# Kernel optimization log

Measured on AMD Instinct MI355X. Metric: run time of the kernel, lower is better.

Reference implementation:

```python
import jax, jax.numpy as jnp
import numpy as np

B, T, I, H = 32, 1024, 512, 512


def setup_inputs() -> dict:
    key = jax.random.key(0)
    ks = jax.random.split(key, 9)
    s = 0.05  # xavier-ish scale for 512-dim layers
    return {
        "x": jax.random.normal(ks[0], (B, T, I), jnp.float32),
        "W_in_0": jax.random.normal(ks[1], (I, H), jnp.float32) * s,
        "b_in_0": jnp.zeros((H,), jnp.float32),
        "W_h_0": jax.random.normal(ks[2], (H, 2 * H), jnp.float32) * s,
        "b_h_0": jnp.zeros((2 * H,), jnp.float32),
        "W_in_1": jax.random.normal(ks[3], (H, H), jnp.float32) * s,
        "b_in_1": jnp.zeros((H,), jnp.float32),
        "W_h_1": jax.random.normal(ks[4], (H, 2 * H), jnp.float32) * s,
        "b_h_1": jnp.zeros((2 * H,), jnp.float32),
    }


def _cell(ti, m_prev, c_prev, W_h, b_h, hid):
    # ti: transformed input [B,H]; gates from previous m (the "hidden")
    gates = m_prev @ W_h + b_h                 # [B,2H]
    retain = jax.nn.sigmoid(gates[:, :hid])
    merge = jax.nn.sigmoid(gates[:, hid:])
    c_next = jnp.tanh(c_prev + retain * ti)
    m_next = (1.0 - merge) * ti + merge * c_next
    return m_next, c_next


def reference(x, W_in_0, b_in_0, W_h_0, b_h_0, W_in_1, b_in_1, W_h_1, b_h_1):
    b, t, _ = x.shape
    hid = W_in_0.shape[1]
    # layer-0 input transform is independent of the recurrence: batch it over time
    ti0_all = jnp.swapaxes(x @ W_in_0 + b_in_0, 0, 1)  # [T,B,H]

    def step(carry, ti0):
        (m0, c0), (m1, c1) = carry
        m0n, c0n = _cell(ti0, m0, c0, W_h_0, b_h_0, hid)
        ti1 = m0n @ W_in_1 + b_in_1
        m1n, c1n = _cell(ti1, m1, c1, W_h_1, b_h_1, hid)
        out_t = jnp.stack([m0n, m1n], axis=1)  # [B,L,H]
        return ((m0n, c0n), (m1n, c1n)), out_t

    z = jnp.zeros((b, hid), x.dtype)
    init = ((z, z), (z, z))
    (h0, h1), outs = jax.lax.scan(step, init, ti0_all)
    output = jnp.swapaxes(outs, 0, 1)  # [B,T,L,H]
    final_c = jnp.stack([h0[1], h1[1]], axis=1)  # [B,L,H]
    con = jnp.broadcast_to(final_c[:, None], output.shape)  # [B,T,L,H]
    return (output, output, con)
```

## Files before the change

### kernel.cpp

```cpp
#include <hip/hip_runtime.h>


#define T_STEPS 1024

typedef __bf16 bf8 __attribute__((ext_vector_type(8)));
typedef float  f4  __attribute__((ext_vector_type(4)));
typedef unsigned u32x4 __attribute__((ext_vector_type(4)));

__device__ __forceinline__ f4 mfma16(bf8 a, bf8 b, f4 c) {
    return __builtin_amdgcn_mfma_f32_16x16x32_bf16(a, b, c, 0, 0, 0);
}
__device__ __forceinline__ float sigf(float x)     { return 1.f / (1.f + __expf(-x)); }
__device__ __forceinline__ float tanhfast(float x) { return 1.f - 2.f / (1.f + __expf(2.f * x)); }
__device__ __forceinline__ unsigned pack2(float lo, float hi) {
    union { __bf16 h; unsigned short u; } a, b;
    a.h = (__bf16)lo; b.h = (__bf16)hi;
    return ((unsigned)b.u << 16) | (unsigned)a.u;
}
__device__ __forceinline__ void wait_lds_ge(int* p, int tgt) {
    while (__hip_atomic_load(p, __ATOMIC_ACQUIRE, __HIP_MEMORY_SCOPE_WORKGROUP) < tgt)
        __builtin_amdgcn_s_sleep(1);
}
__device__ __forceinline__ void set_lds(int* p, int v) {
    __hip_atomic_store(p, v, __ATOMIC_RELEASE, __HIP_MEMORY_SCOPE_WORKGROUP);
}


__global__ __launch_bounds__(256) void k_init(const float* __restrict__ x,
                                              const float* __restrict__ w_in0,
                                              __bf16* __restrict__ xbf,
                                              __bf16* __restrict__ w0hi,
                                              __bf16* __restrict__ w0lo,
                                              unsigned* __restrict__ ws)
{
    size_t id = (size_t)blockIdx.x * 256 + threadIdx.x;
    size_t gs = (size_t)gridDim.x * 256;
    for (size_t i = id; i < 33024; i += gs) ws[i] = 0u;
    for (size_t i = id; i < (size_t)16777216; i += gs) {
        size_t r = i >> 9, c = i & 511;
        size_t b = r & 31, t = r >> 5;
        xbf[i] = (__bf16)x[(((b << 10) + t) << 9) + c];
    }
    for (size_t i = id; i < (size_t)262144; i += gs) {
        size_t n = i >> 9, k = i & 511;
        float v = w_in0[(k << 9) + n];
        __bf16 h = (__bf16)v;
        w0hi[i] = h;
        w0lo[i] = (__bf16)(v - (float)h);
    }
}

__global__ __launch_bounds__(256) void k_pregemm(const __bf16* __restrict__ xbf,
                                                 const __bf16* __restrict__ w0hi,
                                                 const __bf16* __restrict__ w0lo,
                                                 const float* __restrict__ b_in0,
                                                 float* __restrict__ ti0)
{
    int tid = threadIdx.x, lane = tid & 63, wid = tid >> 6;
    int wg = blockIdx.x;
    int mbase = (wg & 511) * 64 + wid * 16;
    int nbase = (wg >> 9) * 128;
    int col = lane & 15, kgrp = lane >> 4;
    f4 acc[8];
#pragma unroll
    for (int i = 0; i < 8; ++i) acc[i] = (f4){0.f, 0.f, 0.f, 0.f};
    const __bf16* ap = xbf + (size_t)(mbase + col) * 512 + kgrp * 8;
    for (int kk = 0; kk < 16; ++kk) {
        bf8 a = *reinterpret_cast<const bf8*>(ap + kk * 32);
        const __bf16* wb = w0hi + (size_t)(nbase + col) * 512 + kk * 32 + kgrp * 8;
        const __bf16* wl = w0lo + (size_t)(nbase + col) * 512 + kk * 32 + kgrp * 8;
#pragma unroll
        for (int ct = 0; ct < 8; ++ct) {
            bf8 bh = *reinterpret_cast<const bf8*>(wb + (size_t)ct * 16 * 512);
            bf8 bl = *reinterpret_cast<const bf8*>(wl + (size_t)ct * 16 * 512);
            acc[ct] = mfma16(a, bh, acc[ct]);
            acc[ct] = mfma16(a, bl, acc[ct]);
        }
    }
#pragma unroll
    for (int ct = 0; ct < 8; ++ct) {
        int c = nbase + ct * 16 + col;
        float bias = b_in0[c];
#pragma unroll
        for (int r = 0; r < 4; ++r) {
            int row = mbase + kgrp * 4 + r;
            ti0[(size_t)row * 512 + c] = acc[ct][r] + bias;
        }
    }
}

__global__ __launch_bounds__(192, 1) void k_recur(
    const float* __restrict__ wh0, const float* __restrict__ bh0g,
    const float* __restrict__ win1, const float* __restrict__ bin1g,
    const float* __restrict__ wh1, const float* __restrict__ bh1g,
    const float* __restrict__ ti0,
    float* __restrict__ out,
    unsigned* __restrict__ ws)
{
    __shared__ __bf16 sW[9][8192];
    __shared__ float  sTi1[2][256];
    __shared__ float  sMn[2][256];
    __shared__ float  sB[5][16];
    __shared__ int    sAready, sAout, sBdone, sCdone;

    int tid = threadIdx.x, lane = tid & 63, wid = tid >> 6;
    int wg = blockIdx.x;
    int rank  = wg & 31;
    int mhalf = wg >> 5;

    unsigned* flagsA = ws + mhalf * 64;
    unsigned* flagsB = ws + 128 + mhalf * 64;
    unsigned* ring0d = ws + 256;
    unsigned* ring1d = ws + 256 + 16384;
    float* fc = (float*)(ws + 33024);

    int h0 = rank * 16;
    int col = lane & 15, kgrp = lane >> 4;
    int rbrow = mhalf * 16;

    for (int i = tid; i < 8192; i += 192) {
        int cl = i & 15, k = i >> 4;
        int sw = (cl * 512 + k) ^ ((cl & 7) << 3);
        float v0r = wh0[(size_t)k * 1024 + h0 + cl];
        float v0m = wh0[(size_t)k * 1024 + 512 + h0 + cl];
        float v1r = wh1[(size_t)k * 1024 + h0 + cl];
        float v1m = wh1[(size_t)k * 1024 + 512 + h0 + cl];
        float vt  = win1[(size_t)k * 512 + h0 + cl];
        __bf16 a;
        a = (__bf16)v0r; sW[0][sw] = a; sW[1][sw] = (__bf16)(v0r - (float)a);
        a = (__bf16)v0m; sW[2][sw] = a; sW[3][sw] = (__bf16)(v0m - (float)a);
        a = (__bf16)v1r; sW[4][sw] = a; sW[5][sw] = (__bf16)(v1r - (float)a);
        a = (__bf16)v1m; sW[6][sw] = a; sW[7][sw] = (__bf16)(v1m - (float)a);
        sW[8][sw] = (__bf16)vt;
    }
    if (tid < 16) {
        sB[0][tid] = bh0g[h0 + tid];
        sB[1][tid] = bh0g[512 + h0 + tid];
        sB[2][tid] = bh1g[h0 + tid];
        sB[3][tid] = bh1g[512 + h0 + tid];
        sB[4][tid] = bin1g[h0 + tid];
    }
    if (tid == 0) { sAready = -1; sAout = -1; sBdone = -1; sCdone = -1; }
    __syncthreads();

    float cs[4] = {0.f, 0.f, 0.f, 0.f};

    if (wid == 0) {
#pragma unroll 1
        for (int ph = 0; ph <= T_STEPS; ++ph) {
            float t0v[4] = {0.f, 0.f, 0.f, 0.f};
            if (ph < T_STEPS) {
#pragma unroll
                for (int r = 0; r < 4; ++r)
                    t0v[r] = ti0[((size_t)ph * 32 + rbrow + kgrp * 4 + r) * 512 + h0 + col];
            }
            if (ph > 0) {
                const unsigned tgt = (unsigned)ph;
                const unsigned* fp = flagsA + (lane & 31);
                while (true) {
                    unsigned v = __hip_atomic_load(fp, __ATOMIC_RELAXED,
                                                   __HIP_MEMORY_SCOPE_AGENT);
                    if (__ballot(v >= tgt) == ~0ull) break;
                    __builtin_amdgcn_s_sleep(1);
                }
                __builtin_amdgcn_sched_barrier(0);
            }
            u32x4 au[16];
            {
                const unsigned* rp = ring0d + ((ph + 1) & 1) * 8192 + (rbrow + col) * 256 + kgrp * 4;
#pragma unroll
                for (int kk = 0; kk < 16; ++kk)
                    asm volatile("global_load_dwordx4 %0, %1, off sc1"
                                 : "=v"(au[kk]) : "v"(rp + kk * 16));
                asm volatile("s_waitcnt vmcnt(0)" ::: "memory");
            }
            f4 accR = {0.f, 0.f, 0.f, 0.f};
            f4 accM = {0.f, 0.f, 0.f, 0.f};
            f4 accT = {0.f, 0.f, 0.f, 0.f};
#pragma unroll
            for (int kk = 0; kk < 16; ++kk) {
                union { u32x4 u; bf8 v; } A;
                A.u = au[kk];
                int e = (col * 512 + kk * 32 + kgrp * 8) ^ ((col & 7) << 3);
                accR = mfma16(A.v, *reinterpret_cast<const bf8*>(&sW[0][e]), accR);
                accR = mfma16(A.v, *reinterpret_cast<const bf8*>(&sW[1][e]), accR);
                accM = mfma16(A.v, *reinterpret_cast<const bf8*>(&sW[2][e]), accM);
                accM = mfma16(A.v, *reinterpret_cast<const bf8*>(&sW[3][e]), accM);
                accT = mfma16(A.v, *reinterpret_cast<const bf8*>(&sW[8][e]), accT);
            }
            wait_lds_ge(&sBdone, ph - 2);
#pragma unroll
            for (int r = 0; r < 4; ++r)
                sTi1[ph & 1][(kgrp * 4 + r) * 16 + col] = accT[r] + sB[4][col];
            if (lane == 0) set_lds(&sAready, ph);

            if (ph < T_STEPS) {
                float mn[4];
#pragma unroll
                for (int r = 0; r < 4; ++r) {
                    float retain = sigf(accR[r] + sB[0][col]);
                    float merge  = sigf(accM[r] + sB[1][col]);
                    float cv = tanhfast(cs[r] + retain * t0v[r]);
                    cs[r] = cv;
                    mn[r] = (1.f - merge) * t0v[r] + merge * cv;
                }
#pragma unroll
                for (int r = 0; r < 4; ++r) {
                    float hi = __shfl_xor(mn[r], 1, 64);
                    if (!(col & 1)) {
                        int grow = rbrow + kgrp * 4 + r;
                        __hip_atomic_store(&ring0d[(ph & 1) * 8192 + grow * 256 + rank * 8 + (col >> 1)],
                                           pack2(mn[r], hi), __ATOMIC_RELAXED,
                                           __HIP_MEMORY_SCOPE_AGENT);
                    }
                }
                asm volatile("s_waitcnt vmcnt(0)" ::: "memory");
                if (lane == 0)
                    __hip_atomic_store(&flagsA[rank], (unsigned)(ph + 1), __ATOMIC_RELAXED,
                                       __HIP_MEMORY_SCOPE_AGENT);
                wait_lds_ge(&sCdone, ph - 2);
#pragma unroll
                for (int r = 0; r < 4; ++r)
                    sMn[ph & 1][(kgrp * 4 + r) * 16 + col] = mn[r];
                if (lane == 0) set_lds(&sAout, ph);
            }
        }
#pragma unroll
        for (int r = 0; r < 4; ++r) {
            int b = rbrow + kgrp * 4 + r;
            fc[((size_t)b * 2 + 0) * 512 + h0 + col] = cs[r];
        }
    } else if (wid == 1) {
#pragma unroll 1
        for (int ph = 1; ph <= T_STEPS; ++ph) {
            if (ph >= 2) {
                const unsigned tgt = (unsigned)(ph - 1);
                const unsigned* fp = flagsB + (lane & 31);
                while (true) {
                    unsigned v = __hip_atomic_load(fp, __ATOMIC_RELAXED,
                                                   __HIP_MEMORY_SCOPE_AGENT);
                    if (__ballot(v >= tgt) == ~0ull) break;
                    __builtin_amdgcn_s_sleep(1);
                }
                __builtin_amdgcn_sched_barrier(0);
            }
            u32x4 au[16];
            {
                const unsigned* rp = ring1d + (ph & 1) * 8192 + (rbrow + col) * 256 + kgrp * 4;
#pragma unroll
                for (int kk = 0; kk < 16; ++kk)
                    asm volatile("global_load_dwordx4 %0, %1, off sc1"
                                 : "=v"(au[kk]) : "v"(rp + kk * 16));
                asm volatile("s_waitcnt vmcnt(0)" ::: "memory");
            }
            f4 accR = {0.f, 0.f, 0.f, 0.f};
            f4 accM = {0.f, 0.f, 0.f, 0.f};
#pragma unroll
            for (int kk = 0; kk < 16; ++kk) {
                union { u32x4 u; bf8 v; } A;
                A.u = au[kk];
                int e = (col * 512 + kk * 32 + kgrp * 8) ^ ((col & 7) << 3);
                accR = mfma16(A.v, *reinterpret_cast<const bf8*>(&sW[4][e]), accR);
                accR = mfma16(A.v, *reinterpret_cast<const bf8*>(&sW[5][e]), accR);
                accM = mfma16(A.v, *reinterpret_cast<const bf8*>(&sW[6][e]), accM);
                accM = mfma16(A.v, *reinterpret_cast<const bf8*>(&sW[7][e]), accM);
            }
            wait_lds_ge(&sAready, ph);
            float mn[4];
#pragma unroll
            for (int r = 0; r < 4; ++r) {
                float t1v = sTi1[ph & 1][(kgrp * 4 + r) * 16 + col];
                float retain = sigf(accR[r] + sB[2][col]);
                float merge  = sigf(accM[r] + sB[3][col]);
                float cv = tanhfast(cs[r] + retain * t1v);
                cs[r] = cv;
                mn[r] = (1.f - merge) * t1v + merge * cv;
            }
            if (lane == 0) set_lds(&sBdone, ph);
#pragma unroll
            for (int r = 0; r < 4; ++r) {
                float hi = __shfl_xor(mn[r], 1, 64);
                if (!(col & 1)) {
                    int grow = rbrow + kgrp * 4 + r;
                    __hip_atomic_store(&ring1d[((ph + 1) & 1) * 8192 + grow * 256 + rank * 8 + (col >> 1)],
                                       pack2(mn[r], hi), __ATOMIC_RELAXED,
                                       __HIP_MEMORY_SCOPE_AGENT);
                }
            }
            asm volatile("s_waitcnt vmcnt(0)" ::: "memory");
            if (lane == 0)
                __hip_atomic_store(&flagsB[rank], (unsigned)ph, __ATOMIC_RELAXED,
                                   __HIP_MEMORY_SCOPE_AGENT);
#pragma unroll
            for (int r = 0; r < 4; ++r) {
                int b = rbrow + kgrp * 4 + r;
                size_t ob = ((size_t)b * 1024 + (ph - 1)) * 1024 + 512 + h0 + col;
                __builtin_nontemporal_store(mn[r], out + ob);
                __builtin_nontemporal_store(mn[r], out + (size_t)33554432 + ob);
            }
        }
#pragma unroll
        for (int r = 0; r < 4; ++r) {
            int b = rbrow + kgrp * 4 + r;
            fc[((size_t)b * 2 + 1) * 512 + h0 + col] = cs[r];
        }
    } else {
#pragma unroll 1
        for (int ph = 0; ph < T_STEPS; ++ph) {
            wait_lds_ge(&sAout, ph);
            float mn[4];
#pragma unroll
            for (int r = 0; r < 4; ++r)
                mn[r] = sMn[ph & 1][(kgrp * 4 + r) * 16 + col];
            if (lane == 0) set_lds(&sCdone, ph);
#pragma unroll
            for (int r = 0; r < 4; ++r) {
                int b = rbrow + kgrp * 4 + r;
                size_t ob = ((size_t)b * 1024 + ph) * 1024 + h0 + col;
                __builtin_nontemporal_store(mn[r], out + ob);
                __builtin_nontemporal_store(mn[r], out + (size_t)33554432 + ob);
            }
        }
    }
}

__global__ __launch_bounds__(256) void k_final(const float* __restrict__ fc,
                                               float* __restrict__ seg2)
{
    size_t id = (size_t)blockIdx.x * 256 + threadIdx.x;
    size_t gs = (size_t)gridDim.x * 256;
    for (size_t i = id; i < (size_t)8388608; i += gs) {
        size_t flat = i * 4;
        int h = (int)(flat & 511);
        int l = (int)((flat >> 9) & 1);
        int b = (int)(flat >> 20);
        f4 v = *reinterpret_cast<const f4*>(&fc[((size_t)b * 2 + l) * 512 + h]);
        *reinterpret_cast<f4*>(&seg2[flat]) = v;
    }
}

extern "C" void kernel_launch(void* const* d_in, const int* in_sizes, int n_in,
                              void* d_out, int out_size, void* d_ws, size_t ws_size,
                              hipStream_t stream)
{
    const float* x     = (const float*)d_in[0];
    const float* w_in0 = (const float*)d_in[1];
    const float* b_in0 = (const float*)d_in[2];
    const float* wh0   = (const float*)d_in[3];
    const float* bh0   = (const float*)d_in[4];
    const float* win1  = (const float*)d_in[5];
    const float* bin1  = (const float*)d_in[6];
    const float* wh1   = (const float*)d_in[7];
    const float* bh1   = (const float*)d_in[8];
    float* out = (float*)d_out;

    float*  seg2 = out + (size_t)2 * 33554432;
    float*  ti0  = seg2;
    __bf16* xbf  = (__bf16*)(ti0 + 16777216);
    __bf16* w0hi = xbf + 16777216;
    __bf16* w0lo = w0hi + 262144;

    k_init<<<1024, 256, 0, stream>>>(x, w_in0, xbf, w0hi, w0lo, (unsigned*)d_ws);
    k_pregemm<<<2048, 256, 0, stream>>>(xbf, w0hi, w0lo, b_in0, ti0);
    k_recur<<<64, 192, 0, stream>>>(wh0, bh0, win1, bin1, wh1, bh1, ti0, out,
                                    (unsigned*)d_ws);
    k_final<<<1024, 256, 0, stream>>>((const float*)((unsigned*)d_ws + 33024), seg2);
}
```

Measured before the change: 5.325 ms.

## Replace flag-based inter-block sync with step-tagged ring entries; offload layer-1 stores

Result: slower. 7.572 ms (+42.2%).

```diff
diff --git a/kernel.cpp b/kernel.cpp
--- a/kernel.cpp
+++ b/kernel.cpp
@@ -31,11 +31,11 @@
                                               __bf16* __restrict__ xbf,
                                               __bf16* __restrict__ w0hi,
                                               __bf16* __restrict__ w0lo,
-                                              unsigned* __restrict__ ws)
+                                              unsigned* __restrict__ ringz)
 {
     size_t id = (size_t)blockIdx.x * 256 + threadIdx.x;
     size_t gs = (size_t)gridDim.x * 256;
-    for (size_t i = id; i < 33024; i += gs) ws[i] = 0u;
+    for (size_t i = id; i < 65536; i += gs) ringz[i] = 0u;
     for (size_t i = id; i < (size_t)16777216; i += gs) {
         size_t r = i >> 9, c = i & 511;
         size_t b = r & 31, t = r >> 5;
@@ -89,30 +89,60 @@
     }
 }
 
+__device__ __forceinline__ void pull_ring(const unsigned long long* rp, unsigned tg,
+                                          bf8* afr)
+{
+    while (true) {
+        u32x4 au[32];
+#pragma unroll
+        for (int kk = 0; kk < 16; ++kk) {
+            asm volatile("global_load_dwordx4 %0, %1, off sc1"
+                         : "=v"(au[2 * kk]) : "v"(rp + (size_t)kk * 16));
+            asm volatile("global_load_dwordx4 %0, %1, off sc1"
+                         : "=v"(au[2 * kk + 1]) : "v"(rp + (size_t)kk * 16 + 2));
+        }
+        asm volatile("s_waitcnt vmcnt(0)" ::: "memory");
+        __builtin_amdgcn_sched_barrier(0);
+        unsigned bad = 0;
+#pragma unroll
+        for (int i = 0; i < 32; ++i) bad |= (au[i][1] ^ tg) | (au[i][3] ^ tg);
+        if (__ballot(bad == 0) == ~0ull) {
+#pragma unroll
+            for (int kk = 0; kk < 16; ++kk) {
+                union { u32x4 u; bf8 v; } A;
+                A.u = (u32x4){au[2 * kk][0], au[2 * kk][2],
+                              au[2 * kk + 1][0], au[2 * kk + 1][2]};
+                afr[kk] = A.v;
+            }
+            return;
+        }
+        __builtin_amdgcn_s_sleep(1);
+    }
+}
+
 __global__ __launch_bounds__(192, 1) void k_recur(
     const float* __restrict__ wh0, const float* __restrict__ bh0g,
     const float* __restrict__ win1, const float* __restrict__ bin1g,
     const float* __restrict__ wh1, const float* __restrict__ bh1g,
     const float* __restrict__ ti0,
     float* __restrict__ out,
-    unsigned* __restrict__ ws)
+    float* __restrict__ fc,
+    unsigned long long* __restrict__ ringbase)
 {
     __shared__ __bf16 sW[9][8192];
     __shared__ float  sTi1[2][256];
-    __shared__ float  sMn[2][256];
+    __shared__ float  sMn0[2][256];
+    __shared__ float  sMn1[2][256];
     __shared__ float  sB[5][16];
-    __shared__ int    sAready, sAout, sBdone, sCdone;
+    __shared__ int    sAready, sAout, sB1rdy, sBdone, sCdone;
 
     int tid = threadIdx.x, lane = tid & 63, wid = tid >> 6;
     int wg = blockIdx.x;
     int rank  = wg & 31;
     int mhalf = wg >> 5;
 
-    unsigned* flagsA = ws + mhalf * 64;
-    unsigned* flagsB = ws + 128 + mhalf * 64;
-    unsigned* ring0d = ws + 256;
-    unsigned* ring1d = ws + 256 + 16384;
-    float* fc = (float*)(ws + 33024);
+    unsigned long long* ring0t = ringbase;
+    unsigned long long* ring1t = ringbase + 16384;
 
     int h0 = rank * 16;
     int col = lane & 15, kgrp = lane >> 4;
@@ -140,7 +170,7 @@
         sB[3][tid] = bh1g[512 + h0 + tid];
         sB[4][tid] = bin1g[h0 + tid];
     }
-    if (tid == 0) { sAready = -1; sAout = -1; sBdone = -1; sCdone = -1; }
+    if (tid == 0) { sAready = -1; sAout = -1; sB1rdy = -1; sBdone = -1; sCdone = -1; }
     __syncthreads();
 
     float cs[4] = {0.f, 0.f, 0.f, 0.f};
@@ -154,39 +184,20 @@
                 for (int r = 0; r < 4; ++r)
                     t0v[r] = ti0[((size_t)ph * 32 + rbrow + kgrp * 4 + r) * 512 + h0 + col];
             }
-            if (ph > 0) {
-                const unsigned tgt = (unsigned)ph;
-                const unsigned* fp = flagsA + (lane & 31);
-                while (true) {
-                    unsigned v = __hip_atomic_load(fp, __ATOMIC_RELAXED,
-                                                   __HIP_MEMORY_SCOPE_AGENT);
-                    if (__ballot(v >= tgt) == ~0ull) break;
-                    __builtin_amdgcn_s_sleep(1);
-                }
-                __builtin_amdgcn_sched_barrier(0);
-            }
-            u32x4 au[16];
-            {
-                const unsigned* rp = ring0d + ((ph + 1) & 1) * 8192 + (rbrow + col) * 256 + kgrp * 4;
-#pragma unroll
-                for (int kk = 0; kk < 16; ++kk)
-                    asm volatile("global_load_dwordx4 %0, %1, off sc1"
-                                 : "=v"(au[kk]) : "v"(rp + kk * 16));
-                asm volatile("s_waitcnt vmcnt(0)" ::: "memory");
-            }
+            bf8 afr[16];
+            pull_ring(ring0t + ((ph + 1) & 1) * 8192 + (size_t)(rbrow + col) * 256 + kgrp * 4,
+                      (unsigned)ph, afr);
             f4 accR = {0.f, 0.f, 0.f, 0.f};
             f4 accM = {0.f, 0.f, 0.f, 0.f};
             f4 accT = {0.f, 0.f, 0.f, 0.f};
 #pragma unroll
             for (int kk = 0; kk < 16; ++kk) {
-                union { u32x4 u; bf8 v; } A;
-                A.u = au[kk];
                 int e = (col * 512 + kk * 32 + kgrp * 8) ^ ((col & 7) << 3);
-                accR = mfma16(A.v, *reinterpret_cast<const bf8*>(&sW[0][e]), accR);
-                accR = mfma16(A.v, *reinterpret_cast<const bf8*>(&sW[1][e]), accR);
-                accM = mfma16(A.v, *reinterpret_cast<const bf8*>(&sW[2][e]), accM);
-                accM = mfma16(A.v, *reinterpret_cast<const bf8*>(&sW[3][e]), accM);
-                accT = mfma16(A.v, *reinterpret_cast<const bf8*>(&sW[8][e]), accT);
+                accR = mfma16(afr[kk], *reinterpret_cast<const bf8*>(&sW[0][e]), accR);
+                accR = mfma16(afr[kk], *reinterpret_cast<const bf8*>(&sW[1][e]), accR);
+                accM = mfma16(afr[kk], *reinterpret_cast<const bf8*>(&sW[2][e]), accM);
+                accM = mfma16(afr[kk], *reinterpret_cast<const bf8*>(&sW[3][e]), accM);
+                accT = mfma16(afr[kk], *reinterpret_cast<const bf8*>(&sW[8][e]), accT);
             }
             wait_lds_ge(&sBdone, ph - 2);
 #pragma unroll
@@ -204,24 +215,21 @@
                     cs[r] = cv;
                     mn[r] = (1.f - merge) * t0v[r] + merge * cv;
                 }
+                unsigned tg1 = (unsigned)(ph + 1);
 #pragma unroll
                 for (int r = 0; r < 4; ++r) {
                     float hi = __shfl_xor(mn[r], 1, 64);
                     if (!(col & 1)) {
                         int grow = rbrow + kgrp * 4 + r;
-                        __hip_atomic_store(&ring0d[(ph & 1) * 8192 + grow * 256 + rank * 8 + (col >> 1)],
-                                           pack2(mn[r], hi), __ATOMIC_RELAXED,
-                                           __HIP_MEMORY_SCOPE_AGENT);
+                        unsigned long long w = ((unsigned long long)tg1 << 32) | pack2(mn[r], hi);
+                        __hip_atomic_store(&ring0t[(ph & 1) * 8192 + (size_t)grow * 256 + rank * 8 + (col >> 1)],
+                                           w, __ATOMIC_RELAXED, __HIP_MEMORY_SCOPE_AGENT);
                     }
                 }
-                asm volatile("s_waitcnt vmcnt(0)" ::: "memory");
-                if (lane == 0)
-                    __hip_atomic_store(&flagsA[rank], (unsigned)(ph + 1), __ATOMIC_RELAXED,
-                                       __HIP_MEMORY_SCOPE_AGENT);
                 wait_lds_ge(&sCdone, ph - 2);
 #pragma unroll
                 for (int r = 0; r < 4; ++r)
-                    sMn[ph & 1][(kgrp * 4 + r) * 16 + col] = mn[r];
+                    sMn0[ph & 1][(kgrp * 4 + r) * 16 + col] = mn[r];
                 if (lane == 0) set_lds(&sAout, ph);
             }
         }
@@ -233,71 +241,50 @@
     } else if (wid == 1) {
 #pragma unroll 1
         for (int ph = 1; ph <= T_STEPS; ++ph) {
-            if (ph >= 2) {
-                const unsigned tgt = (unsigned)(ph - 1);
-                const unsigned* fp = flagsB + (lane & 31);
-                while (true) {
-                    unsigned v = __hip_atomic_load(fp, __ATOMIC_RELAXED,
-                                                   __HIP_MEMORY_SCOPE_AGENT);
-                    if (__ballot(v >= tgt) == ~0ull) break;
-                    __builtin_amdgcn_s_sleep(1);
-                }
-                __builtin_amdgcn_sched_barrier(0);
-            }
-            u32x4 au[16];
-            {
-                const unsigned* rp = ring1d + (ph & 1) * 8192 + (rbrow + col) * 256 + kgrp * 4;
-#pragma unroll
-                for (int kk = 0; kk < 16; ++kk)
-                    asm volatile("global_load_dwordx4 %0, %1, off sc1"
-                                 : "=v"(au[kk]) : "v"(rp + kk * 16));
-                asm volatile("s_waitcnt vmcnt(0)" ::: "memory");
-            }
+            bf8 afr[16];
+            pull_ring(ring1t + (ph & 1) * 8192 + (size_t)(rbrow + col) * 256 + kgrp * 4,
+                      (unsigned)(ph - 1), afr);
             f4 accR = {0.f, 0.f, 0.f, 0.f};
             f4 accM = {0.f, 0.f, 0.f, 0.f};
 #pragma unroll
             for (int kk = 0; kk < 16; ++kk) {
-                union { u32x4 u; bf8 v; } A;
-                A.u = au[kk];
                 int e = (col * 512 + kk * 32 + kgrp * 8) ^ ((col & 7) << 3);
-                accR = mfma16(A.v, *reinterpret_cast<const bf8*>(&sW[4][e]), accR);
-                accR = mfma16(A.v, *reinterpret_cast<const bf8*>(&sW[5][e]), accR);
-                accM = mfma16(A.v, *reinterpret_cast<const bf8*>(&sW[6][e]), accM);
-                accM = mfma16(A.v, *reinterpret_cast<const bf8*>(&sW[7][e]), accM);
+                accR = mfma16(afr[kk], *reinterpret_cast<const bf8*>(&sW[4][e]), accR);
+                accR = mfma16(afr[kk], *reinterpret_cast<const bf8*>(&sW[5][e]), accR);
+                accM = mfma16(afr[kk], *reinterpret_cast<const bf8*>(&sW[6][e]), accM);
+                accM = mfma16(afr[kk], *reinterpret_cast<const bf8*>(&sW[7][e]), accM);
             }
             wait_lds_ge(&sAready, ph);
+            float t1v[4];
+#pragma unroll
+            for (int r = 0; r < 4; ++r)
+                t1v[r] = sTi1[ph & 1][(kgrp * 4 + r) * 16 + col];
+            if (lane == 0) set_lds(&sBdone, ph);
             float mn[4];
 #pragma unroll
             for (int r = 0; r < 4; ++r) {
-                float t1v = sTi1[ph & 1][(kgrp * 4 + r) * 16 + col];
                 float retain = sigf(accR[r] + sB[2][col]);
                 float merge  = sigf(accM[r] + sB[3][col]);
-                float cv = tanhfast(cs[r] + retain * t1v);
+                float cv = tanhfast(cs[r] + retain * t1v[r]);
                 cs[r] = cv;
-                mn[r] = (1.f - merge) * t1v + merge * cv;
-            }
-            if (lane == 0) set_lds(&sBdone, ph);
+                mn[r] = (1.f - merge) * t1v[r] + merge * cv;
+            }
+            unsigned tg1 = (unsigned)ph;
 #pragma unroll
             for (int r = 0; r < 4; ++r) {
                 float hi = __shfl_xor(mn[r], 1, 64);
                 if (!(col & 1)) {
                     int grow = rbrow + kgrp * 4 + r;
-                    __hip_atomic_store(&ring1d[((ph + 1) & 1) * 8192 + grow * 256 + rank * 8 + (col >> 1)],
-                                       pack2(mn[r], hi), __ATOMIC_RELAXED,
-                                       __HIP_MEMORY_SCOPE_AGENT);
-                }
-            }
-            asm volatile("s_waitcnt vmcnt(0)" ::: "memory");
-            if (lane == 0)
-                __hip_atomic_store(&flagsB[rank], (unsigned)ph, __ATOMIC_RELAXED,
-                                   __HIP_MEMORY_SCOPE_AGENT);
-#pragma unroll
-            for (int r = 0; r < 4; ++r) {
-                int b = rbrow + kgrp * 4 + r;
-                size_t ob = ((size_t)b * 1024 + (ph - 1)) * 1024 + 512 + h0 + col;
-                __builtin_nontemporal_store(mn[r], out + ob);
-                __builtin_nontemporal_store(mn[r], out + (size_t)33554432 + ob);
-            }
+                    unsigned long long w = ((unsigned long long)tg1 << 32) | pack2(mn[r], hi);
+                    __hip_atomic_store(&ring1t[((ph + 1) & 1) * 8192 + (size_t)grow * 256 + rank * 8 + (col >> 1)],
+                                       w, __ATOMIC_RELAXED, __HIP_MEMORY_SCOPE_AGENT);
+                }
+            }
+            wait_lds_ge(&sCdone, ph - 2);
+#pragma unroll
+            for (int r = 0; r < 4; ++r)
+                sMn1[ph & 1][(kgrp * 4 + r) * 16 + col] = mn[r];
+            if (lane == 0) set_lds(&sB1rdy, ph);
         }
 #pragma unroll
         for (int r = 0; r < 4; ++r) {
@@ -306,19 +293,39 @@
         }
     } else {
 #pragma unroll 1
-        for (int ph = 0; ph < T_STEPS; ++ph) {
-            wait_lds_ge(&sAout, ph);
-            float mn[4];
-#pragma unroll
-            for (int r = 0; r < 4; ++r)
-                mn[r] = sMn[ph & 1][(kgrp * 4 + r) * 16 + col];
+        for (int ph = 0; ph <= T_STEPS; ++ph) {
+            float m0[4], m1[4];
+            bool has0 = (ph < T_STEPS), has1 = (ph >= 1);
+            if (has0) {
+                wait_lds_ge(&sAout, ph);
+#pragma unroll
+                for (int r = 0; r < 4; ++r)
+                    m0[r] = sMn0[ph & 1][(kgrp * 4 + r) * 16 + col];
+            }
+            if (has1) {
+                wait_lds_ge(&sB1rdy, ph);
+#pragma unroll
+                for (int r = 0; r < 4; ++r)
+                    m1[r] = sMn1[ph & 1][(kgrp * 4 + r) * 16 + col];
+            }
             if (lane == 0) set_lds(&sCdone, ph);
-#pragma unroll
-            for (int r = 0; r < 4; ++r) {
-                int b = rbrow + kgrp * 4 + r;
-                size_t ob = ((size_t)b * 1024 + ph) * 1024 + h0 + col;
-                __builtin_nontemporal_store(mn[r], out + ob);
-                __builtin_nontemporal_store(mn[r], out + (size_t)33554432 + ob);
+            if (has0) {
+#pragma unroll
+                for (int r = 0; r < 4; ++r) {
+                    int b = rbrow + kgrp * 4 + r;
+                    size_t ob = ((size_t)b * 1024 + ph) * 1024 + h0 + col;
+                    __builtin_nontemporal_store(m0[r], out + ob);
+                    __builtin_nontemporal_store(m0[r], out + (size_t)33554432 + ob);
+                }
+            }
+            if (has1) {
+#pragma unroll
+                for (int r = 0; r < 4; ++r) {
+                    int b = rbrow + kgrp * 4 + r;
+                    size_t ob = ((size_t)b * 1024 + (ph - 1)) * 1024 + 512 + h0 + col;
+                    __builtin_nontemporal_store(m1[r], out + ob);
+                    __builtin_nontemporal_store(m1[r], out + (size_t)33554432 + ob);
+                }
             }
         }
     }
@@ -359,10 +366,11 @@
     __bf16* xbf  = (__bf16*)(ti0 + 16777216);
     __bf16* w0hi = xbf + 16777216;
     __bf16* w0lo = w0hi + 262144;
-
-    k_init<<<1024, 256, 0, stream>>>(x, w_in0, xbf, w0hi, w0lo, (unsigned*)d_ws);
+    unsigned long long* ringt = (unsigned long long*)(seg2 + 26214400);
+
+    k_init<<<1024, 256, 0, stream>>>(x, w_in0, xbf, w0hi, w0lo, (unsigned*)ringt);
     k_pregemm<<<2048, 256, 0, stream>>>(xbf, w0hi, w0lo, b_in0, ti0);
     k_recur<<<64, 192, 0, stream>>>(wh0, bh0, win1, bin1, wh1, bh1, ti0, out,
-                                    (unsigned*)d_ws);
-    k_final<<<1024, 256, 0, stream>>>((const float*)((unsigned*)d_ws + 33024), seg2);
-}
+                                    (float*)d_ws, ringt);
+    k_final<<<1024, 256, 0, stream>>>((const float*)d_ws, seg2);
+}
```
